# Kernel optimization log

Measured on AMD Instinct MI355X. Metric: run time of the kernel, lower is better.

## Reference

```python
import jax, jax.numpy as jnp
import numpy as np
from jax import lax

SIGMAS = [0.5, 1.0, 2.0, 4.0, 8.0]
FILTER_SIZE = int(4 * SIGMAS[-1] + 1)  # 33
PAD = int(2 * SIGMAS[-1])              # 16
DR = 1.0
C1 = (0.01 * DR) ** 2
C2 = (0.03 * DR) ** 2
ALPHA = 0.025
COMPENSATION = 200.0
LAMBDA_PIXEL = 100.0


def _gauss_2d(size, sigma):
    coords = np.arange(size, dtype=np.float32) - size // 2
    g = np.exp(-coords ** 2 / (2.0 * sigma ** 2))
    g = g / g.sum()
    return np.outer(g, g)  # (size, size)


def _build_g_masks():
    # Shape (15, 1, 33, 33): 3 identical copies per sigma, interleaved as in torch code.
    m = np.zeros((3 * len(SIGMAS), 1, FILTER_SIZE, FILTER_SIZE), dtype=np.float32)
    for idx, s in enumerate(SIGMAS):
        k = _gauss_2d(FILTER_SIZE, s)
        m[3 * idx + 0, 0] = k
        m[3 * idx + 1, 0] = k
        m[3 * idx + 2, 0] = k
    return jnp.asarray(m)


def _gconv(t, w):
    # Grouped conv, groups=3 (torch semantics: out channel j in group j // (O/3),
    # group g reads input channel g). 'same' padding via explicit PAD.
    return lax.conv_general_dilated(
        t, w, window_strides=(1, 1), padding=[(PAD, PAD), (PAD, PAD)],
        feature_group_count=3, dimension_numbers=('NCHW', 'OIHW', 'NCHW'))


def setup_inputs() -> dict:
    key = jax.random.key(0)
    k1, k2, k3 = jax.random.split(key, 3)
    x = jax.random.normal(k1, (8, 3, 512, 512), dtype=jnp.float32)
    y = jax.random.normal(k2, (8, 3, 512, 512), dtype=jnp.float32)
    disc_out = jax.random.normal(k3, (8, 1, 62, 62), dtype=jnp.float32)
    return {"x": x, "y": y, "disc_out": disc_out, "g_masks": _build_g_masks()}


def reference(x, y, disc_out, g_masks):
    # denormalize: tanh output [-1,1] -> [0,1]
    x = x * 0.5 + 0.5
    y = y * 0.5 + 0.5

    mux = _gconv(x, g_masks)          # (B, 15, H, W)
    muy = _gconv(y, g_masks)
    mux2 = mux * mux
    muy2 = muy * muy
    muxy = mux * muy
    sigmax2 = _gconv(x * x, g_masks) - mux2
    sigmay2 = _gconv(y * y, g_masks) - muy2
    sigmaxy = _gconv(x * y, g_masks) - muxy

    l = (2.0 * muxy + C1) / (mux2 + muy2 + C1)
    cs = (2.0 * sigmaxy + C2) / (sigmax2 + sigmay2 + C2)

    lM = l[:, -1] * l[:, -2] * l[:, -3]       # (B, H, W)
    PIcs = jnp.prod(cs, axis=1)               # (B, H, W)
    loss_ms_ssim = 1.0 - lM * PIcs

    loss_l1 = jnp.abs(x - y)                  # (B, 3, H, W)
    # narrow(0, -3, 3) -> last 3 filters (sigma=8), grouped conv then channel mean
    gaussian_l1 = _gconv(loss_l1, g_masks[-3:]).mean(axis=1)  # (B, H, W)

    loss_mix = ALPHA * loss_ms_ssim + (1.0 - ALPHA) * gaussian_l1 / DR
    loss_mix = COMPENSATION * loss_mix

    # GeneratorLoss: lambda_pixel * L1(x, y) + MSE(disc_out, 1)
    gen_loss = LAMBDA_PIXEL * jnp.mean(jnp.abs(x - y)) + jnp.mean((disc_out - 1.0) ** 2)

    return (loss_mix.mean() + gen_loss) / 2.0
```

## Files before the change

### kernel.cpp

```cpp
#include <hip/hip_runtime.h>
#include <stdint.h>


#define TILE 32
#define HALO 16
#define SSTR 72
#define PLN  (64 * SSTR)
#define PTPLN (32 * SSTR)
#define NT   256

#define C1c 1.0e-4f
#define C2c 9.0e-4f

typedef short bf16x8 __attribute__((ext_vector_type(8)));
typedef float f32x4  __attribute__((ext_vector_type(4)));
typedef unsigned short ush;

constexpr double cexp(double xx) {
  if (xx < -700.0) return 0.0;
  const double ln2 = 0.6931471805599453, il2 = 1.4426950408889634;
  double kd = xx * il2;
  long long k = (long long)(kd + (kd >= 0 ? 0.5 : -0.5));
  double r = xx - (double)k * ln2;
  double t = 1.0, s = 1.0;
  for (int i = 1; i <= 22; ++i) { t *= r / (double)i; s += t; }
  double p = 1.0, base = (k >= 0) ? 2.0 : 0.5;
  long long n = (k >= 0) ? k : -k;
  while (n) { if (n & 1) p *= base; base *= base; n >>= 1; }
  return s * p;
}
constexpr float gsi(double sigma) {
  double inv = 1.0 / (2.0 * sigma * sigma);
  double s = 0.0;
  for (int k = -16; k <= 16; ++k) s += cexp(-(double)(k * k) * inv);
  return (float)(1.0 / s);
}
constexpr float SI05 = gsi(0.5), SI10 = gsi(1.0), SI20 = gsi(2.0),
                SI40 = gsi(4.0), SI80 = gsi(8.0);

__device__ __forceinline__ unsigned f2bf_pk(float lo, float hi) {
  union { float f; unsigned u; } a, b; a.f = lo; b.f = hi;
  return __builtin_amdgcn_perm(b.u + 0x8000u, a.u + 0x8000u, 0x07060302u);
}
__device__ __forceinline__ ush f2bf1(float f) {
  union { float f; unsigned u; } c; c.f = f;
  return (ush)((c.u + 0x8000u) >> 16);
}

struct WFrag {
  bf16x8 h[2][2];
};

template<int SIG>
__device__ __forceinline__ void build_wm(ush* __restrict__ WM,
                                         const float (*__restrict__ wf5)[40],
                                         int tid, int wave, int lane,
                                         WFrag& W) {
  __syncthreads();
  #pragma unroll
  for (int i = 0; i < 8; ++i) {
    const int idx = i * 256 + tid;
    const int m = idx >> 6, k = idx & 63;
    const int t = k - m;
    const int tc = t < 0 ? 0 : (t > 32 ? 32 : t);
    float v = wf5[SIG][tc];
    v = (t >= 0 && t <= 32) ? v : 0.f;
    WM[m * SSTR + k] = f2bf1(v);
  }
  __syncthreads();
  const int l16 = lane & 15, quad = lane >> 4;
  #pragma unroll
  for (int t = 0; t < 2; ++t)
    #pragma unroll
    for (int c = 0; c < 2; ++c)
      W.h[t][c] = *(const bf16x8*)(WM + (t * 16 + l16) * SSTR + quad * 8 + 32 * c);
}

template<int NQ>
__device__ __forceinline__ void conv_pass(const bf16x8 (&A)[NQ][2],
                                          const WFrag& W,
                                          const ush* __restrict__ WM,
                                          ush* __restrict__ PT,
                                          int wave, int lane, f32x4* V) {
  const int l16 = lane & 15, quad = lane >> 4;
  const int m0 = wave * 16;
  #pragma unroll
  for (int q = 0; q < NQ; ++q) {
    #pragma unroll
    for (int nt = 0; nt < 2; ++nt) {
      f32x4 acc = {0.f, 0.f, 0.f, 0.f};
      acc = __builtin_amdgcn_mfma_f32_16x16x32_bf16(A[q][0], W.h[nt][0], acc, 0, 0, 0);
      acc = __builtin_amdgcn_mfma_f32_16x16x32_bf16(A[q][1], W.h[nt][1], acc, 0, 0, 0);
      uint2 u;
      u.x = f2bf_pk(acc[0], acc[1]);
      u.y = f2bf_pk(acc[2], acc[3]);
      *(uint2*)(PT + q * PTPLN + (nt * 16 + l16) * SSTR + m0 + quad * 4) = u;
    }
  }
  const ush* wvp = WM + ((wave >> 1) * 16 + l16) * SSTR + quad * 8;
  const bf16x8 wv0 = *(const bf16x8*)wvp;
  const bf16x8 wv1 = *(const bf16x8*)(wvp + 32);
  __syncthreads();
  const int n0 = (wave & 1) * 16;
  #pragma unroll
  for (int q = 0; q < NQ; ++q) {
    const ush* pp = PT + q * PTPLN + (n0 + l16) * SSTR + quad * 8;
    const bf16x8 b0 = *(const bf16x8*)pp;
    const bf16x8 b1 = *(const bf16x8*)(pp + 32);
    f32x4 acc = {0.f, 0.f, 0.f, 0.f};
    acc = __builtin_amdgcn_mfma_f32_16x16x32_bf16(wv0, b0, acc, 0, 0, 0);
    acc = __builtin_amdgcn_mfma_f32_16x16x32_bf16(wv1, b1, acc, 0, 0, 0);
    V[q] = acc;
  }
}

__device__ __forceinline__ void ssim_fold(const f32x4* V, int mult, bool last,
                                          float* PIcs) {
  #pragma unroll
  for (int r = 0; r < 4; ++r) {
    const float mux = V[0][r], muy = V[1][r];
    const float A = mux * muy;
    const float Bq = mux * mux + muy * muy;
    const float S = V[2][r] + V[3][r] - Bq;
    const float sxy = V[4][r] - A;
    const float cs = (2.f * sxy + C2c) * __builtin_amdgcn_rcpf(S + C2c);
    float p = cs;
    if (mult >= 2) p *= cs;
    if (mult >= 3) p *= cs;
    if (last) {
      const float l = (2.f * A + C1c) * __builtin_amdgcn_rcpf(Bq + C1c);
      p *= l * l * l;
    }
    PIcs[r] *= p;
  }
}

__global__ __launch_bounds__(NT)
void msssim_fused_kernel(const float* __restrict__ x, const float* __restrict__ y,
                         const float* __restrict__ disc,
                         float* __restrict__ partials) {
  __shared__ ush XQ[2 * PLN];
  __shared__ ush PT[5 * PTPLN];
  __shared__ ush WM[32 * SSTR];
  __shared__ float wf5[5][40];
  __shared__ float red[12];

  const int tid = threadIdx.x;
  const int wave = tid >> 6, lane = tid & 63;
  const int bx = blockIdx.x, by = blockIdx.y, b = blockIdx.z;
  const int x0 = bx * TILE - HALO, y0 = by * TILE - HALO;
  const int blk = (b * 16 + by) * 16 + bx;

  float d2 = 0.f;
  { const int di = blk * 16 + tid;
    if (tid < 16 && di < 8 * 62 * 62) { const float dd = disc[di] - 1.f; d2 = dd * dd; } }

  if (tid < 165) {
    const int sig = tid / 33;
    const int k = tid - sig * 33;
    const float d = (float)(k - 16);
    float inv, si;
    if (sig == 0)      { inv = 2.0f;       si = SI05; }
    else if (sig == 1) { inv = 0.5f;       si = SI10; }
    else if (sig == 2) { inv = 0.125f;     si = SI20; }
    else if (sig == 3) { inv = 0.03125f;   si = SI40; }
    else               { inv = 0.0078125f; si = SI80; }
    wf5[sig][k] = __expf(-d * d * inv) * si;
  }

  const int sr = tid >> 4;
  const int sc = (tid & 15) * 4;

  float4 PX[4], PY[4];
  auto issue_loads = [&](int ch) {
    const float* __restrict__ xs = x + (size_t)(b * 3 + ch) * 262144;
    const float* __restrict__ ys = y + (size_t)(b * 3 + ch) * 262144;
    #pragma unroll
    for (int it = 0; it < 4; ++it) {
      const int r = it * 16 + sr;
      const int gy = y0 + r, gx = x0 + sc;
      const bool rowok = (gy >= 0) && (gy < 512);
      if (rowok && gx >= 0 && gx <= 508) {
        PX[it] = *(const float4*)(xs + gy * 512 + gx);
        PY[it] = *(const float4*)(ys + gy * 512 + gx);
      } else {
        float tx[4], ty[4];
        #pragma unroll
        for (int e = 0; e < 4; ++e) {
          const int g = gx + e;
          const bool ok = rowok && (g >= 0) && (g < 512);
          tx[e] = ok ? xs[gy * 512 + g] : 0.f;
          ty[e] = ok ? ys[gy * 512 + g] : 0.f;
        }
        PX[it] = make_float4(tx[0], tx[1], tx[2], tx[3]);
        PY[it] = make_float4(ty[0], ty[1], ty[2], ty[3]);
      }
    }
  };

  float PIcs[4] = {1.f, 1.f, 1.f, 1.f};
  float sad[4][4];
  #pragma unroll
  for (int it = 0; it < 4; ++it)
    #pragma unroll
    for (int e = 0; e < 4; ++e) sad[it][e] = 0.f;

  issue_loads(0);

  auto stage = [&]() {
    #pragma unroll
    for (int it = 0; it < 4; ++it) {
      const int r = it * 16 + sr;
      float xv[4] = {PX[it].x, PX[it].y, PX[it].z, PX[it].w};
      float yv[4] = {PY[it].x, PY[it].y, PY[it].z, PY[it].w};
      #pragma unroll
      for (int e = 0; e < 4; ++e) {
        xv[e] = fmaf(xv[e], 0.5f, 0.5f);
        yv[e] = fmaf(yv[e], 0.5f, 0.5f);
        sad[it][e] += fabsf(xv[e] - yv[e]);
      }
      const int off = r * SSTR + sc;
      *(uint2*)(XQ + 0 * PLN + off) = make_uint2(f2bf_pk(xv[0], xv[1]), f2bf_pk(xv[2], xv[3]));
      *(uint2*)(XQ + 1 * PLN + off) = make_uint2(f2bf_pk(yv[0], yv[1]), f2bf_pk(yv[2], yv[3]));
    }
  };

  f32x4 V[5];
  WFrag W;
  bf16x8 AF[5][2];

  auto load_derive = [&]() {
    const int l16 = lane & 15, quad = lane >> 4;
    const ush* xp = XQ + (wave * 16 + l16) * SSTR + quad * 8;
    AF[0][0] = *(const bf16x8*)xp;
    AF[0][1] = *(const bf16x8*)(xp + 32);
    AF[1][0] = *(const bf16x8*)(xp + PLN);
    AF[1][1] = *(const bf16x8*)(xp + PLN + 32);
    #pragma unroll
    for (int c = 0; c < 2; ++c) {
      float xf[8], yf[8];
      #pragma unroll
      for (int e = 0; e < 8; ++e) {
        union { unsigned u; float f; } ax, ay;
        ax.u = ((unsigned)(ush)AF[0][c][e]) << 16;
        ay.u = ((unsigned)(ush)AF[1][c][e]) << 16;
        xf[e] = ax.f; yf[e] = ay.f;
      }
      union { unsigned u[4]; bf16x8 v; } w2, w3, w4;
      #pragma unroll
      for (int p = 0; p < 4; ++p) {
        w2.u[p] = f2bf_pk(xf[2*p] * xf[2*p], xf[2*p+1] * xf[2*p+1]);
        w3.u[p] = f2bf_pk(yf[2*p] * yf[2*p], yf[2*p+1] * yf[2*p+1]);
        w4.u[p] = f2bf_pk(xf[2*p] * yf[2*p], xf[2*p+1] * yf[2*p+1]);
      }
      AF[2][c] = w2.v; AF[3][c] = w3.v; AF[4][c] = w4.v;
    }
  };

  stage();
  issue_loads(1);
  build_wm<0>(WM, wf5, tid, wave, lane, W);
  load_derive();
  conv_pass<5>(AF, W, WM, PT, wave, lane, V);
  ssim_fold(V, 3, false, PIcs);
  build_wm<1>(WM, wf5, tid, wave, lane, W);
  conv_pass<5>(AF, W, WM, PT, wave, lane, V);
  ssim_fold(V, 2, false, PIcs);

  stage();
  issue_loads(2);
  __syncthreads();
  load_derive();
  conv_pass<5>(AF, W, WM, PT, wave, lane, V);
  ssim_fold(V, 1, false, PIcs);
  build_wm<2>(WM, wf5, tid, wave, lane, W);
  conv_pass<5>(AF, W, WM, PT, wave, lane, V);
  ssim_fold(V, 3, false, PIcs);
  build_wm<3>(WM, wf5, tid, wave, lane, W);
  conv_pass<5>(AF, W, WM, PT, wave, lane, V);
  ssim_fold(V, 1, false, PIcs);

  stage();
  __syncthreads();
  load_derive();
  conv_pass<5>(AF, W, WM, PT, wave, lane, V);
  ssim_fold(V, 2, false, PIcs);
  build_wm<4>(WM, wf5, tid, wave, lane, W);
  conv_pass<5>(AF, W, WM, PT, wave, lane, V);
  ssim_fold(V, 3, true, PIcs);

  #pragma unroll
  for (int it = 0; it < 4; ++it) {
    const int off = (it * 16 + sr) * SSTR + sc;
    *(uint2*)(XQ + off) =
        make_uint2(f2bf_pk(sad[it][0], sad[it][1]), f2bf_pk(sad[it][2], sad[it][3]));
  }
  __syncthreads();
  bf16x8 SF[1][2];
  {
    const ush* sp = XQ + (wave * 16 + (lane & 15)) * SSTR + (lane >> 4) * 8;
    SF[0][0] = *(const bf16x8*)sp;
    SF[0][1] = *(const bf16x8*)(sp + 32);
  }
  f32x4 V1[1];
  conv_pass<1>(SF, W, WM, PT, wave, lane, V1);

  float absacc = 0.f;
  if (sc >= 16 && sc < 48) {
    #pragma unroll
    for (int it = 1; it <= 2; ++it)
      #pragma unroll
      for (int e = 0; e < 4; ++e) absacc += sad[it][e];
  }

  float mixsum = 0.f;
  #pragma unroll
  for (int r = 0; r < 4; ++r) {
    const float ssim = 1.f - PIcs[r];
    mixsum += 200.f * (0.025f * ssim + 0.975f * (V1[0][r] * (1.f / 3.f)));
  }

  #pragma unroll
  for (int off = 32; off > 0; off >>= 1) {
    mixsum += __shfl_down(mixsum, off);
    absacc += __shfl_down(absacc, off);
    d2     += __shfl_down(d2, off);
  }
  if (lane == 0) { red[wave] = mixsum; red[4 + wave] = absacc; red[8 + wave] = d2; }
  __syncthreads();
  if (tid == 0) {
    float m = 0.f, a = 0.f, d = 0.f;
    #pragma unroll
    for (int i = 0; i < 4; ++i) { m += red[i]; a += red[4 + i]; d += red[8 + i]; }
    partials[3 * blk + 0] = m;
    partials[3 * blk + 1] = a;
    partials[3 * blk + 2] = d;
  }
}

__global__ __launch_bounds__(512)
void msssim_final_kernel(const float* __restrict__ partials,
                         float* __restrict__ out) {
  __shared__ float red[24];
  const int tid = threadIdx.x;
  float m = 0.f, a = 0.f, d2 = 0.f;
  for (int j = tid; j < 2048; j += 512) {
    m  += partials[3 * j + 0];
    a  += partials[3 * j + 1];
    d2 += partials[3 * j + 2];
  }
  #pragma unroll
  for (int off = 32; off > 0; off >>= 1) {
    m  += __shfl_down(m, off);
    a  += __shfl_down(a, off);
    d2 += __shfl_down(d2, off);
  }
  const int wave = tid >> 6, lane = tid & 63;
  if (lane == 0) { red[wave] = m; red[8 + wave] = a; red[16 + wave] = d2; }
  __syncthreads();
  if (tid == 0) {
    float sm = 0.f, sa = 0.f, sd = 0.f;
    #pragma unroll
    for (int i = 0; i < 8; ++i) { sm += red[i]; sa += red[8 + i]; sd += red[16 + i]; }
    const float mix_mean  = sm / (8.f * 512.f * 512.f);
    const float abs_mean  = sa / (8.f * 3.f * 512.f * 512.f);
    const float disc_mean = sd / (8.f * 62.f * 62.f);
    out[0] = 0.5f * (mix_mean + 100.f * abs_mean + disc_mean);
  }
}

extern "C" void kernel_launch(void* const* d_in, const int* in_sizes, int n_in,
                              void* d_out, int out_size, void* d_ws, size_t ws_size,
                              hipStream_t stream) {
  const float* x    = (const float*)d_in[0];
  const float* y    = (const float*)d_in[1];
  const float* disc = (const float*)d_in[2];
  float* partials = (float*)d_ws;
  dim3 grid(16, 16, 8);
  msssim_fused_kernel<<<grid, NT, 0, stream>>>(x, y, disc, partials);
  msssim_final_kernel<<<1, 512, 0, stream>>>(partials, (float*)d_out);
}
```

Baseline: 143.9 us.

## Alias staging and partial-transpose LDS buffers to cut shared memory footprint

The separate XQ input-staging buffer and PT partial-result buffer are merged into one aliased LDS region, with the SAD staging placed at an offset inside it. Extra barriers are added so staging, derive, and conv phases do not overwrite each other's data. The vertical-pass weights are now taken from the register-held W fragments instead of being reloaded from LDS. The intent is to lower LDS use per block so more blocks fit per CU, at the cost of additional __syncthreads calls.

```diff
diff --git a/kernel.cpp b/kernel.cpp
--- a/kernel.cpp
+++ b/kernel.cpp
@@ -79,7 +79,6 @@
 template<int NQ>
 __device__ __forceinline__ void conv_pass(const bf16x8 (&A)[NQ][2],
                                           const WFrag& W,
-                                          const ush* __restrict__ WM,
                                           ush* __restrict__ PT,
                                           int wave, int lane, f32x4* V) {
   const int l16 = lane & 15, quad = lane >> 4;
@@ -97,9 +96,8 @@
       *(uint2*)(PT + q * PTPLN + (nt * 16 + l16) * SSTR + m0 + quad * 4) = u;
     }
   }
-  const ush* wvp = WM + ((wave >> 1) * 16 + l16) * SSTR + quad * 8;
-  const bf16x8 wv0 = *(const bf16x8*)wvp;
-  const bf16x8 wv1 = *(const bf16x8*)(wvp + 32);
+  const bf16x8 wv0 = (wave & 2) ? W.h[1][0] : W.h[0][0];
+  const bf16x8 wv1 = (wave & 2) ? W.h[1][1] : W.h[0][1];
   __syncthreads();
   const int n0 = (wave & 1) * 16;
   #pragma unroll
@@ -139,11 +137,14 @@
 void msssim_fused_kernel(const float* __restrict__ x, const float* __restrict__ y,
                          const float* __restrict__ disc,
                          float* __restrict__ partials) {
-  __shared__ ush XQ[2 * PLN];
-  __shared__ ush PT[5 * PTPLN];
+  __shared__ ush REGION[5 * PTPLN];
   __shared__ ush WM[32 * SSTR];
   __shared__ float wf5[5][40];
   __shared__ float red[12];
+
+  ush* const XQ  = REGION;
+  ush* const PTB = REGION;
+  ush* const SADP = REGION + PTPLN;
 
   const int tid = threadIdx.x;
   const int wave = tid >> 6, lane = tid & 63;
@@ -259,51 +260,57 @@
 
   stage();
   issue_loads(1);
+  __syncthreads();
+  load_derive();
   build_wm<0>(WM, wf5, tid, wave, lane, W);
-  load_derive();
-  conv_pass<5>(AF, W, WM, PT, wave, lane, V);
+  conv_pass<5>(AF, W, PTB, wave, lane, V);
   ssim_fold(V, 3, false, PIcs);
   build_wm<1>(WM, wf5, tid, wave, lane, W);
-  conv_pass<5>(AF, W, WM, PT, wave, lane, V);
+  conv_pass<5>(AF, W, PTB, wave, lane, V);
   ssim_fold(V, 2, false, PIcs);
 
+  __syncthreads();
   stage();
   issue_loads(2);
   __syncthreads();
   load_derive();
-  conv_pass<5>(AF, W, WM, PT, wave, lane, V);
+  __syncthreads();
+  conv_pass<5>(AF, W, PTB, wave, lane, V);
   ssim_fold(V, 1, false, PIcs);
   build_wm<2>(WM, wf5, tid, wave, lane, W);
-  conv_pass<5>(AF, W, WM, PT, wave, lane, V);
+  conv_pass<5>(AF, W, PTB, wave, lane, V);
   ssim_fold(V, 3, false, PIcs);
   build_wm<3>(WM, wf5, tid, wave, lane, W);
-  conv_pass<5>(AF, W, WM, PT, wave, lane, V);
+  conv_pass<5>(AF, W, PTB, wave, lane, V);
   ssim_fold(V, 1, false, PIcs);
 
+  __syncthreads();
   stage();
   __syncthreads();
   load_derive();
-  conv_pass<5>(AF, W, WM, PT, wave, lane, V);
+  __syncthreads();
+  conv_pass<5>(AF, W, PTB, wave, lane, V);
   ssim_fold(V, 2, false, PIcs);
   build_wm<4>(WM, wf5, tid, wave, lane, W);
-  conv_pass<5>(AF, W, WM, PT, wave, lane, V);
+  conv_pass<5>(AF, W, PTB, wave, lane, V);
   ssim_fold(V, 3, true, PIcs);
 
+  __syncthreads();
   #pragma unroll
   for (int it = 0; it < 4; ++it) {
     const int off = (it * 16 + sr) * SSTR + sc;
-    *(uint2*)(XQ + off) =
+    *(uint2*)(SADP + off) =
         make_uint2(f2bf_pk(sad[it][0], sad[it][1]), f2bf_pk(sad[it][2], sad[it][3]));
   }
   __syncthreads();
   bf16x8 SF[1][2];
   {
-    const ush* sp = XQ + (wave * 16 + (lane & 15)) * SSTR + (lane >> 4) * 8;
+    const ush* sp = SADP + (wave * 16 + (lane & 15)) * SSTR + (lane >> 4) * 8;
     SF[0][0] = *(const bf16x8*)sp;
     SF[0][1] = *(const bf16x8*)(sp + 32);
   }
   f32x4 V1[1];
-  conv_pass<1>(SF, W, WM, PT, wave, lane, V1);
+  conv_pass<1>(SF, W, PTB, wave, lane, V1);
 
   float absacc = 0.f;
   if (sc >= 16 && sc < 48) {
```

Measured after the change: 144.6 us. About the same (+0.5%).
